# Kernel tuning notes

Hardware: AMD Instinct MI355X
Metric: run time of the kernel (lower is better)

## Reference

```python
import jax, jax.numpy as jnp
import numpy as np
import math

F = 64        # num_features (multiplicity of each irrep)
N = 16000     # nodes
E = 256000    # edges (avg_num_neighbors = 16)
S = 4         # num_species
DE = 32       # scalar edge feature dim (radial basis)
W = 128       # interaction_mlp_width
AVG_NEIGH = 16.0
SQ2 = math.sqrt(2.0)
SQ3 = math.sqrt(3.0)


def setup_inputs() -> dict:
    key = jax.random.key(0)
    ks = jax.random.split(key, 32)
    def nrm(k, shape, scale=1.0):
        return jax.random.normal(k, shape, dtype=jnp.float32) * scale
    inp = {}
    # forward args
    inp["vectors"] = nrm(ks[0], (E, 1, 3))
    inp["lengths"] = jax.random.uniform(ks[1], (E, 1), dtype=jnp.float32)
    inp["node_s"] = nrm(ks[2], (N, F))            # 64x0e part of node_feats
    inp["node_v"] = nrm(ks[3], (N, F, 3))         # 64x1o part of node_feats
    inp["scalar_edge_feats"] = nrm(ks[4], (E, DE))
    inp["node_specie"] = jax.random.randint(ks[5], (N,), 0, S)
    inp["senders"] = jax.random.randint(ks[6], (E,), 0, N)
    inp["receivers"] = jax.random.randint(ks[7], (E,), 0, N)
    # parameters (e3nn Linear = per-irrep channel mixing, fan-in normalized; bias only on 0e)
    inp["W_up_s"] = nrm(ks[8], (F, F), F ** -0.5); inp["b_up_s"] = jnp.zeros((F,), jnp.float32)
    inp["W_up_v"] = nrm(ks[9], (F, F), F ** -0.5)
    din = 2 * F + DE + 1
    inp["mlp_W1"] = nrm(ks[10], (din, W), din ** -0.5); inp["mlp_b1"] = jnp.zeros((W,), jnp.float32)
    inp["mlp_W2"] = nrm(ks[11], (W, W), W ** -0.5); inp["mlp_b2"] = jnp.zeros((W,), jnp.float32)
    inp["mlp_W3"] = nrm(ks[12], (W, 3 * F), W ** -0.5); inp["mlp_b3"] = jnp.zeros((3 * F,), jnp.float32)
    inp["W_dn_s"] = nrm(ks[13], (F, F), F ** -0.5); inp["b_dn_s"] = jnp.zeros((F,), jnp.float32)
    inp["W_dn_v"] = nrm(ks[14], (2 * F, F), (2 * F) ** -0.5)
    # symmetric contraction weights (per species, per channel); correlation=2
    inp["w_sc_s"] = nrm(ks[15], (S, 3, F), 3 ** -0.5)   # paths to 0e: x0, x0^2, (x1.x1)/sqrt3
    inp["w_sc_v"] = nrm(ks[16], (S, 2, F), 2 ** -0.5)   # paths to 1o: x1, x0*x1
    inp["W_pb_s"] = nrm(ks[17], (F, F), F ** -0.5); inp["b_pb_s"] = jnp.zeros((F,), jnp.float32)
    inp["W_pb_v"] = nrm(ks[18], (F, F), F ** -0.5)
    inp["W_r1_s"] = nrm(ks[19], (F, 2 * F), F ** -0.5); inp["b_r1_s"] = jnp.zeros((2 * F,), jnp.float32)
    inp["W_r1_v"] = nrm(ks[20], (F, F), F ** -0.5)
    inp["W_r2_s"] = nrm(ks[21], (F, 1), F ** -0.5); inp["b_r2"] = jnp.zeros((1,), jnp.float32)
    inp["W_r2_v"] = nrm(ks[22], (F, 1), F ** -0.5)
    return inp


def reference(vectors, lengths, node_s, node_v, scalar_edge_feats, node_specie,
              senders, receivers,
              W_up_s, b_up_s, W_up_v,
              mlp_W1, mlp_b1, mlp_W2, mlp_b2, mlp_W3, mlp_b3,
              W_dn_s, b_dn_s, W_dn_v,
              w_sc_s, w_sc_v, W_pb_s, b_pb_s, W_pb_v,
              W_r1_s, b_r1_s, W_r1_v, W_r2_s, b_r2, W_r2_v):
    n = node_s.shape[0]
    # --- spherical harmonics, sh_irreps='1o', component normalization, normalize=False ---
    edge_v = SQ3 * vectors[:, 0, :]                              # [E,3]

    # --- InteractionBlock: linear_up ---
    h_s = node_s @ W_up_s + b_up_s                               # [N,F]
    h_v = jnp.einsum('nfi,fg->ngi', node_v, W_up_v)              # [N,F,3]

    # --- MessagePassingConvolution ---
    m_s = h_s[senders]                                           # [E,F] 0e
    m_v = h_v[senders]                                           # [E,F,3] 1o
    # tensor product with edge 1o, filtered to 0e+1o (unitary CG):
    tp_s = jnp.einsum('efi,ei->ef', m_v, edge_v) / SQ3           # 1o x 1o -> 0e  [E,F]
    tp_v1 = m_s[:, :, None] * edge_v[:, None, :]                 # 0e x 1o -> 1o  [E,F,3]
    tp_v2 = jnp.cross(m_v, edge_v[:, None, :]) / SQ2             # 1o x 1o -> 1o  [E,F,3]
    # scalar MLP mix (one scalar weight per output irrep = 3F)
    mlp_in = jnp.concatenate([m_s, h_s[receivers], scalar_edge_feats, lengths], axis=1)
    h = jax.nn.silu(mlp_in @ mlp_W1 + mlp_b1)
    h = jax.nn.silu(h @ mlp_W2 + mlp_b2)
    mix = h @ mlp_W3 + mlp_b3                                    # [E,3F]
    mix_s, mix_v1, mix_v2 = mix[:, :F], mix[:, F:2 * F], mix[:, 2 * F:]
    tp_s = tp_s * mix_s
    tp_v = jnp.concatenate([tp_v1 * mix_v1[:, :, None], tp_v2 * mix_v2[:, :, None]], axis=1)  # [E,2F,3]
    # scatter-add to receivers, normalize by avg_num_neighbors
    agg_s = jax.ops.segment_sum(tp_s, receivers, num_segments=n) / AVG_NEIGH   # [N,F]
    agg_v = jax.ops.segment_sum(tp_v, receivers, num_segments=n) / AVG_NEIGH   # [N,2F,3]
    # linear_down
    f_s = agg_s @ W_dn_s + b_dn_s                                # [N,F]
    f_v = jnp.einsum('nfi,fg->ngi', agg_v, W_dn_v)               # [N,F,3]

    # --- EquivariantProductBasisBlock: symmetric contraction (correlation=2), per-species ---
    ws = w_sc_s[node_specie]                                     # [N,3,F]
    wv = w_sc_v[node_specie]                                     # [N,2,F]
    vv = jnp.sum(f_v * f_v, axis=-1) / SQ3                       # 1o (x) 1o -> 0e, symmetric
    sc_s = ws[:, 0] * f_s + ws[:, 1] * (f_s * f_s) + ws[:, 2] * vv           # [N,F]
    sc_v = wv[:, 0][:, :, None] * f_v + wv[:, 1][:, :, None] * (f_s[:, :, None] * f_v)  # [N,F,3]
    p_s = sc_s @ W_pb_s + b_pb_s                                 # node_feats 0e out
    p_v = jnp.einsum('nfi,fg->ngi', sc_v, W_pb_v)                # node_feats 1o out

    # --- NonLinearReadoutBlock: linear to (2F x 0e + F x 1o), gate, linear to 1x0e+1x1o ---
    r_s = p_s @ W_r1_s + b_r1_s                                  # [N,2F]
    r_v = jnp.einsum('nfi,fg->ngi', p_v, W_r1_v)                 # [N,F,3]
    act = jax.nn.silu(r_s[:, :F])
    gates = jax.nn.silu(r_s[:, F:])
    g_v = gates[:, :, None] * r_v                                # gated vectors
    out_s = act @ W_r2_s + b_r2                                  # [N,1]  0e output
    out_v = jnp.einsum('nfi,fo->noi', g_v, W_r2_v)               # [N,1,3] 1o output
    return out_s, out_v, p_s, p_v
```

## Files before the change

kernel.cpp:

```cpp
#include <hip/hip_runtime.h>

typedef short bf16x8 __attribute__((ext_vector_type(8)));
typedef float f32x4  __attribute__((ext_vector_type(4)));
typedef unsigned short ushort_t;

__device__ __forceinline__ float silu(float x) {
    float t = __expf(-x);
    return x * __builtin_amdgcn_rcpf(1.f + t);
}

__device__ __forceinline__ ushort_t f2bs(float x) {
    union { float f; unsigned int u; } v; v.f = x;
    unsigned int r = v.u + 0x7FFF + ((v.u >> 16) & 1);
    return (ushort_t)(r >> 16);
}
__device__ __forceinline__ ushort_t f2bs_t(float x) {
    union { float f; unsigned int u; } v; v.f = x;
    return (ushort_t)(v.u >> 16);
}
__device__ __forceinline__ float bs2f(ushort_t x) {
    union { unsigned int u; float f; } v; v.u = ((unsigned int)x) << 16; return v.f;
}

constexpr int N_   = 16000;
constexpr int E_   = 256000;
constexpr int Fd   = 64;

constexpr float SQ3f    = 1.7320508075688772f;
constexpr float INV_SQ3 = 0.5773502691896258f;
constexpr float INV_SQ2 = 0.7071067811865476f;
constexpr float INV_AVG = 0.0625f;

constexpr int OFF_OS = 0;
constexpr int OFF_OV = N_;
constexpr int OFF_PS = OFF_OV + 3 * N_;
constexpr int OFF_PV = OFF_PS + N_ * Fd;

constexpr int W1P_SZ = 6 * 8 * 512;
constexpr int W2P_SZ = 4 * 8 * 512;
constexpr int W3P_SZ = 4 * 12 * 512;

__global__ __launch_bounds__(256) void pack_kernel(
    const float* __restrict__ W1, const float* __restrict__ W2,
    const float* __restrict__ W3,
    ushort_t* __restrict__ W1p, ushort_t* __restrict__ W2p,
    ushort_t* __restrict__ W3p)
{
    int idx = blockIdx.x * 256 + threadIdx.x;
    if (idx < W1P_SZ) {
        int j = idx & 7, lane = (idx >> 3) & 63, tile = idx >> 9;
        int c = tile >> 3, t = tile & 7;
        int k = c * 32 + (lane >> 4) * 8 + j;
        int n = t * 16 + (lane & 15);
        W1p[idx] = f2bs(k < 161 ? W1[k * 128 + n] : 0.f);
    } else if (idx < W1P_SZ + W2P_SZ) {
        int q = idx - W1P_SZ;
        int j = q & 7, lane = (q >> 3) & 63, tile = q >> 9;
        int c = tile >> 3, t = tile & 7;
        int k = c * 32 + (lane >> 4) * 8 + j;
        int n = t * 16 + (lane & 15);
        W2p[q] = f2bs(W2[k * 128 + n]);
    } else {
        int q = idx - W1P_SZ - W2P_SZ;
        int j = q & 7, lane = (q >> 3) & 63, tile = q >> 9;
        int c = tile / 12, t = tile % 12;
        int k = c * 32 + (lane >> 4) * 8 + j;
        int n = t * 16 + (lane & 15);
        W3p[q] = f2bs(W3[k * 192 + n]);
    }
}

__global__ __launch_bounds__(64, 4) void up_kernel(
    const float* __restrict__ node_s, const float* __restrict__ node_v,
    const float* __restrict__ W_up_s, const float* __restrict__ b_up_s,
    const float* __restrict__ W_up_v,
    const int* __restrict__ receivers, int* __restrict__ cnt,
    ushort_t* __restrict__ hs_bf, float* __restrict__ h_v)
{
    __shared__ float ns[4][64];
    __shared__ float nv[4][64][3];
    const int n0 = blockIdx.x * 4;
    const int g  = threadIdx.x;

    {
        int e = blockIdx.x * 64 + g;
        atomicAdd(&cnt[receivers[e]], 1);
    }

    #pragma unroll
    for (int j = 0; j < 4; j++) ns[j][g] = node_s[(n0 + j) * 64 + g];
    for (int idx = g; idx < 4 * 192; idx += 64) {
        int j = idx / 192, r = idx - j * 192;
        nv[j][r / 3][r % 3] = node_v[(size_t)n0 * 192 + idx];
    }
    __syncthreads();

    float as[4], a0[4], a1[4], a2[4];
    float bb = b_up_s[g];
    #pragma unroll
    for (int j = 0; j < 4; j++) { as[j] = bb; a0[j] = a1[j] = a2[j] = 0.f; }
    #pragma unroll 4
    for (int f = 0; f < 64; f++) {
        float wss = W_up_s[f * 64 + g];
        float wv  = W_up_v[f * 64 + g];
        #pragma unroll
        for (int j = 0; j < 4; j++) {
            as[j] += ns[j][f] * wss;
            a0[j] += nv[j][f][0] * wv;
            a1[j] += nv[j][f][1] * wv;
            a2[j] += nv[j][f][2] * wv;
        }
    }
    #pragma unroll
    for (int j = 0; j < 4; j++) {
        hs_bf[(n0 + j) * 64 + g] = f2bs(as[j]);
        h_v[(n0 + j) * 192 + 0 * 64 + g] = a0[j];
        h_v[(n0 + j) * 192 + 1 * 64 + g] = a1[j];
        h_v[(n0 + j) * 192 + 2 * 64 + g] = a2[j];
    }
}

__global__ __launch_bounds__(1024) void scan_kernel(
    const int* __restrict__ cnt, int* __restrict__ base, int* __restrict__ cursor)
{
    __shared__ int part[1024];
    const int t = threadIdx.x;
    int v[16];
    int s = 0;
    if (t < 1000) {
        const int4* c4 = (const int4*)(cnt + t * 16);
        #pragma unroll
        for (int q = 0; q < 4; q++) {
            int4 w = c4[q];
            v[q * 4 + 0] = w.x; v[q * 4 + 1] = w.y;
            v[q * 4 + 2] = w.z; v[q * 4 + 3] = w.w;
            s += w.x + w.y + w.z + w.w;
        }
    }
    part[t] = s;
    __syncthreads();
    for (int off = 1; off < 1024; off <<= 1) {
        int u = (t >= off) ? part[t - off] : 0;
        __syncthreads();
        part[t] += u;
        __syncthreads();
    }
    if (t < 1000) {
        int run = part[t] - s;
        int b[16];
        #pragma unroll
        for (int i = 0; i < 16; i++) { b[i] = run; run += v[i]; }
        int4* bb = (int4*)(base + t * 16);
        int4* cc = (int4*)(cursor + t * 16);
        #pragma unroll
        for (int q = 0; q < 4; q++) {
            int4 w = { b[q * 4], b[q * 4 + 1], b[q * 4 + 2], b[q * 4 + 3] };
            bb[q] = w;
            cc[q] = w;
        }
    }
}

__global__ __launch_bounds__(256, 3) void edge_mlp_kernel(
    const float* __restrict__ lengths, const float* __restrict__ sef,
    const int* __restrict__ senders, const int* __restrict__ receivers,
    const float* __restrict__ b1f, const float* __restrict__ b2f,
    const float* __restrict__ b3f,
    const ushort_t* __restrict__ hs_bf,
    const ushort_t* __restrict__ W1p, const ushort_t* __restrict__ W2p,
    const ushort_t* __restrict__ W3p,
    int* __restrict__ cursor, int* __restrict__ sorted_eid,
    ushort_t* __restrict__ tpx)
{
    __shared__ ushort_t Als[64 * 200];
    __shared__ ushort_t Hs[64 * 136];

    const int tid  = threadIdx.x;
    const int wave = tid >> 6, lane = tid & 63;
    const int quad = lane >> 4, l4 = lane & 15;
    const int e0   = blockIdx.x * 64;

    if (tid < 64) {
        int e = e0 + tid;
        int p = atomicAdd(&cursor[receivers[e]], 1);
        sorted_eid[p] = e;
    }

    {
        const int e  = tid & 63;
        const int ge = e0 + e;
        const int snd = senders[ge];
        const int rcv = receivers[ge];
        for (int c = tid >> 6; c < 24; c += 4) {
            bf16x8 v;
            if (c < 8) {
                v = *(const bf16x8*)(hs_bf + snd * 64 + c * 8);
            } else if (c < 16) {
                v = *(const bf16x8*)(hs_bf + rcv * 64 + (c - 8) * 8);
            } else if (c < 20) {
                const float4 s0 = *(const float4*)(sef + (size_t)ge * 32 + (c - 16) * 8);
                const float4 s1 = *(const float4*)(sef + (size_t)ge * 32 + (c - 16) * 8 + 4);
                v[0] = (short)f2bs(s0.x); v[1] = (short)f2bs(s0.y);
                v[2] = (short)f2bs(s0.z); v[3] = (short)f2bs(s0.w);
                v[4] = (short)f2bs(s1.x); v[5] = (short)f2bs(s1.y);
                v[6] = (short)f2bs(s1.z); v[7] = (short)f2bs(s1.w);
            } else if (c == 20) {
                v = (bf16x8){0,0,0,0,0,0,0,0};
                v[0] = (short)f2bs(lengths[ge]);
            } else {
                v = (bf16x8){0,0,0,0,0,0,0,0};
            }
            *(bf16x8*)(&Als[e * 200 + c * 8]) = v;
        }
    }
    __syncthreads();

    const bf16x8* B1 = (const bf16x8*)W1p;
    const bf16x8* B2 = (const bf16x8*)W2p;
    const bf16x8* B3 = (const bf16x8*)W3p;

    {
        f32x4 acc[2][4];
        #pragma unroll
        for (int ti = 0; ti < 2; ti++)
            #pragma unroll
            for (int m = 0; m < 4; m++) acc[ti][m] = (f32x4){0,0,0,0};
        #pragma unroll
        for (int c = 0; c < 6; c++) {
            bf16x8 b0 = B1[(c * 8 + wave * 2 + 0) * 64 + lane];
            bf16x8 b1 = B1[(c * 8 + wave * 2 + 1) * 64 + lane];
            #pragma unroll
            for (int m = 0; m < 4; m++) {
                bf16x8 a = *(const bf16x8*)(&Als[(m * 16 + l4) * 200 + c * 32 + quad * 8]);
                acc[0][m] = __builtin_amdgcn_mfma_f32_16x16x32_bf16(a, b0, acc[0][m], 0, 0, 0);
                acc[1][m] = __builtin_amdgcn_mfma_f32_16x16x32_bf16(a, b1, acc[1][m], 0, 0, 0);
            }
        }
        #pragma unroll
        for (int ti = 0; ti < 2; ti++) {
            int t = wave * 2 + ti;
            float bb = b1f[t * 16 + l4];
            #pragma unroll
            for (int m = 0; m < 4; m++)
                #pragma unroll
                for (int r = 0; r < 4; r++)
                    Hs[(m * 16 + quad * 4 + r) * 136 + t * 16 + l4] =
                        f2bs_t(silu(acc[ti][m][r] + bb));
        }
    }
    __syncthreads();

    {
        f32x4 acc[2][4];
        #pragma unroll
        for (int ti = 0; ti < 2; ti++)
            #pragma unroll
            for (int m = 0; m < 4; m++) acc[ti][m] = (f32x4){0,0,0,0};
        #pragma unroll
        for (int c = 0; c < 4; c++) {
            bf16x8 b0 = B2[(c * 8 + wave * 2 + 0) * 64 + lane];
            bf16x8 b1 = B2[(c * 8 + wave * 2 + 1) * 64 + lane];
            #pragma unroll
            for (int m = 0; m < 4; m++) {
                bf16x8 a = *(const bf16x8*)(&Hs[(m * 16 + l4) * 136 + c * 32 + quad * 8]);
                acc[0][m] = __builtin_amdgcn_mfma_f32_16x16x32_bf16(a, b0, acc[0][m], 0, 0, 0);
                acc[1][m] = __builtin_amdgcn_mfma_f32_16x16x32_bf16(a, b1, acc[1][m], 0, 0, 0);
            }
        }
        #pragma unroll
        for (int ti = 0; ti < 2; ti++) {
            int t = wave * 2 + ti;
            float bb = b2f[t * 16 + l4];
            #pragma unroll
            for (int m = 0; m < 4; m++)
                #pragma unroll
                for (int r = 0; r < 4; r++)
                    Als[(m * 16 + quad * 4 + r) * 136 + t * 16 + l4] =
                        f2bs_t(silu(acc[ti][m][r] + bb));
        }
    }
    __syncthreads();

    {
        f32x4 acc[3][4];
        #pragma unroll
        for (int ti = 0; ti < 3; ti++)
            #pragma unroll
            for (int m = 0; m < 4; m++) acc[ti][m] = (f32x4){0,0,0,0};
        #pragma unroll
        for (int c = 0; c < 4; c++) {
            bf16x8 b0 = B3[(c * 12 + wave * 3 + 0) * 64 + lane];
            bf16x8 b1 = B3[(c * 12 + wave * 3 + 1) * 64 + lane];
            bf16x8 b2 = B3[(c * 12 + wave * 3 + 2) * 64 + lane];
            #pragma unroll
            for (int m = 0; m < 4; m++) {
                bf16x8 a = *(const bf16x8*)(&Als[(m * 16 + l4) * 136 + c * 32 + quad * 8]);
                acc[0][m] = __builtin_amdgcn_mfma_f32_16x16x32_bf16(a, b0, acc[0][m], 0, 0, 0);
                acc[1][m] = __builtin_amdgcn_mfma_f32_16x16x32_bf16(a, b1, acc[1][m], 0, 0, 0);
                acc[2][m] = __builtin_amdgcn_mfma_f32_16x16x32_bf16(a, b2, acc[2][m], 0, 0, 0);
            }
        }
        #pragma unroll
        for (int ti = 0; ti < 3; ti++) {
            int t = wave * 3 + ti;
            float bb = b3f[t * 16 + l4];
            #pragma unroll
            for (int m = 0; m < 4; m++)
                #pragma unroll
                for (int r = 0; r < 4; r++)
                    tpx[(size_t)(e0 + m * 16 + quad * 4 + r) * 192 + t * 16 + l4] =
                        f2bs(acc[ti][m][r] + bb);
        }
    }
}

__global__ __launch_bounds__(256, 2) void node_fused_kernel(
    const int* __restrict__ base, const int* __restrict__ cnt,
    const int* __restrict__ sorted_eid, const int* __restrict__ senders,
    const float* __restrict__ vectors,
    const ushort_t* __restrict__ tpx,
    const ushort_t* __restrict__ hs_bf, const float* __restrict__ h_v,
    const int* __restrict__ specie,
    const float* __restrict__ W_dn_s, const float* __restrict__ b_dn_s,
    const float* __restrict__ W_dn_v,
    const float* __restrict__ w_sc_s, const float* __restrict__ w_sc_v,
    const float* __restrict__ W_pb_s, const float* __restrict__ b_pb_s,
    const float* __restrict__ W_pb_v,
    const float* __restrict__ W_r1_s, const float* __restrict__ b_r1_s,
    const float* __restrict__ W_r1_v,
    const float* __restrict__ W_r2_s, const float* __restrict__ b_r2,
    const float* __restrict__ W_r2_v,
    float* __restrict__ out)
{
    __shared__ float as_l[4][64];
    __shared__ float av_l[4][128][3];
    __shared__ float scs[4][64];
    __shared__ float scv[4][64][3];
    __shared__ float ps_[4][64];
    __shared__ float pv_[4][64][3];
    __shared__ int   eids[4][64];

    const int tid = threadIdx.x;
    const int w   = tid >> 6;
    const int g   = tid & 63;
    const int n   = blockIdx.x * 4 + w;

    const int b = base[n];
    const int c = cnt[n];
    float accSa = 0.f, accSb = 0.f;
    float a10a = 0.f, a11a = 0.f, a12a = 0.f;
    float a20a = 0.f, a21a = 0.f, a22a = 0.f;
    float a10b = 0.f, a11b = 0.f, a12b = 0.f;
    float a20b = 0.f, a21b = 0.f, a22b = 0.f;

    for (int done = 0; done < c; done += 64) {
        int m = min(64, c - done);
        if (g < m) eids[w][g] = sorted_eid[b + done + g];
        int i = 0;
        for (; i + 1 < m; i += 2) {
            const int e1 = eids[w][i];
            const int e2 = eids[w][i + 1];
            const int se1 = senders[e1];
            const int se2 = senders[e2];
            const float ev10 = SQ3f * vectors[e1 * 3 + 0];
            const float ev11 = SQ3f * vectors[e1 * 3 + 1];
            const float ev12 = SQ3f * vectors[e1 * 3 + 2];
            const float ev20 = SQ3f * vectors[e2 * 3 + 0];
            const float ev21 = SQ3f * vectors[e2 * 3 + 1];
            const float ev22 = SQ3f * vectors[e2 * 3 + 2];
            const float m10 = h_v[(size_t)se1 * 192 + 0 * 64 + g];
            const float m11 = h_v[(size_t)se1 * 192 + 1 * 64 + g];
            const float m12 = h_v[(size_t)se1 * 192 + 2 * 64 + g];
            const float m20 = h_v[(size_t)se2 * 192 + 0 * 64 + g];
            const float m21 = h_v[(size_t)se2 * 192 + 1 * 64 + g];
            const float m22 = h_v[(size_t)se2 * 192 + 2 * 64 + g];
            const float ms1 = bs2f(hs_bf[se1 * 64 + g]);
            const float ms2 = bs2f(hs_bf[se2 * 64 + g]);
            const ushort_t* r1 = tpx + (size_t)e1 * 192;
            const ushort_t* r2 = tpx + (size_t)e2 * 192;
            const float c10 = bs2f(r1[g]), c11 = bs2f(r1[64 + g]), c12 = bs2f(r1[128 + g]);
            const float c20 = bs2f(r2[g]), c21 = bs2f(r2[64 + g]), c22 = bs2f(r2[128 + g]);

            accSa += (m10 * ev10 + m11 * ev11 + m12 * ev12) * c10;
            accSb += (m20 * ev20 + m21 * ev21 + m22 * ev22) * c20;
            float k1a = ms1 * c11, k1b = ms2 * c21;
            a10a += k1a * ev10; a11a += k1a * ev11; a12a += k1a * ev12;
            a10b += k1b * ev20; a11b += k1b * ev21; a12b += k1b * ev22;
            a20a += (m11 * ev12 - m12 * ev11) * c12;
            a21a += (m12 * ev10 - m10 * ev12) * c12;
            a22a += (m10 * ev11 - m11 * ev10) * c12;
            a20b += (m21 * ev22 - m22 * ev21) * c22;
            a21b += (m22 * ev20 - m20 * ev22) * c22;
            a22b += (m20 * ev21 - m21 * ev20) * c22;
        }
        if (i < m) {
            const int e1 = eids[w][i];
            const int se1 = senders[e1];
            const float ev10 = SQ3f * vectors[e1 * 3 + 0];
            const float ev11 = SQ3f * vectors[e1 * 3 + 1];
            const float ev12 = SQ3f * vectors[e1 * 3 + 2];
            const float m10 = h_v[(size_t)se1 * 192 + 0 * 64 + g];
            const float m11 = h_v[(size_t)se1 * 192 + 1 * 64 + g];
            const float m12 = h_v[(size_t)se1 * 192 + 2 * 64 + g];
            const float ms1 = bs2f(hs_bf[se1 * 64 + g]);
            const ushort_t* r1 = tpx + (size_t)e1 * 192;
            const float c10 = bs2f(r1[g]), c11 = bs2f(r1[64 + g]), c12 = bs2f(r1[128 + g]);
            accSa += (m10 * ev10 + m11 * ev11 + m12 * ev12) * c10;
            float k1a = ms1 * c11;
            a10a += k1a * ev10; a11a += k1a * ev11; a12a += k1a * ev12;
            a20a += (m11 * ev12 - m12 * ev11) * c12;
            a21a += (m12 * ev10 - m10 * ev12) * c12;
            a22a += (m10 * ev11 - m11 * ev10) * c12;
        }
    }
    as_l[w][g] = (accSa + accSb) * (INV_SQ3 * INV_AVG);
    av_l[w][g][0] = (a10a + a10b) * INV_AVG;
    av_l[w][g][1] = (a11a + a11b) * INV_AVG;
    av_l[w][g][2] = (a12a + a12b) * INV_AVG;
    av_l[w][64 + g][0] = (a20a + a20b) * (INV_SQ2 * INV_AVG);
    av_l[w][64 + g][1] = (a21a + a21b) * (INV_SQ2 * INV_AVG);
    av_l[w][64 + g][2] = (a22a + a22b) * (INV_SQ2 * INV_AVG);

    float f_s = b_dn_s[g];
    #pragma unroll 8
    for (int f = 0; f < 64; f++) f_s += as_l[w][f] * W_dn_s[f * 64 + g];
    float fv0 = 0.f, fv1 = 0.f, fv2 = 0.f;
    #pragma unroll 8
    for (int f = 0; f < 128; f++) {
        float wt = W_dn_v[f * 64 + g];
        fv0 += av_l[w][f][0] * wt;
        fv1 += av_l[w][f][1] * wt;
        fv2 += av_l[w][f][2] * wt;
    }

    float vv = (fv0 * fv0 + fv1 * fv1 + fv2 * fv2) * INV_SQ3;
    int sp = specie[n];
    float ws0 = w_sc_s[sp * 192 + 0 * 64 + g];
    float ws1 = w_sc_s[sp * 192 + 1 * 64 + g];
    float ws2 = w_sc_s[sp * 192 + 2 * 64 + g];
    float wv0 = w_sc_v[sp * 128 + 0 * 64 + g];
    float wv1 = w_sc_v[sp * 128 + 1 * 64 + g];
    float sc_s = ws0 * f_s + ws1 * f_s * f_s + ws2 * vv;
    float kv = wv0 + wv1 * f_s;
    scs[w][g] = sc_s;
    scv[w][g][0] = kv * fv0;
    scv[w][g][1] = kv * fv1;
    scv[w][g][2] = kv * fv2;

    float p_s = b_pb_s[g];
    float pv0 = 0.f, pv1 = 0.f, pv2 = 0.f;
    #pragma unroll 8
    for (int f = 0; f < 64; f++) {
        float wps = W_pb_s[f * 64 + g];
        p_s += scs[w][f] * wps;
        float wpv = W_pb_v[f * 64 + g];
        pv0 += scv[w][f][0] * wpv;
        pv1 += scv[w][f][1] * wpv;
        pv2 += scv[w][f][2] * wpv;
    }
    ps_[w][g] = p_s;
    pv_[w][g][0] = pv0; pv_[w][g][1] = pv1; pv_[w][g][2] = pv2;

    out[OFF_PS + n * 64 + g] = p_s;
    out[OFF_PV + (size_t)n * 192 + g * 3 + 0] = pv0;
    out[OFF_PV + (size_t)n * 192 + g * 3 + 1] = pv1;
    out[OFF_PV + (size_t)n * 192 + g * 3 + 2] = pv2;

    float r0 = b_r1_s[g];
    float r1 = b_r1_s[g + 64];
    float rv0 = 0.f, rv1 = 0.f, rv2 = 0.f;
    #pragma unroll 8
    for (int f = 0; f < 64; f++) {
        float p = ps_[w][f];
        r0 += p * W_r1_s[f * 128 + g];
        r1 += p * W_r1_s[f * 128 + g + 64];
        float wrv = W_r1_v[f * 64 + g];
        rv0 += pv_[w][f][0] * wrv;
        rv1 += pv_[w][f][1] * wrv;
        rv2 += pv_[w][f][2] * wrv;
    }
    float act  = silu(r0);
    float gate = silu(r1);
    float o_s = act * W_r2_s[g];
    float wr2v = W_r2_v[g];
    float ov0 = gate * rv0 * wr2v;
    float ov1 = gate * rv1 * wr2v;
    float ov2 = gate * rv2 * wr2v;

    #pragma unroll
    for (int off = 32; off > 0; off >>= 1) {
        o_s += __shfl_down(o_s, off);
        ov0 += __shfl_down(ov0, off);
        ov1 += __shfl_down(ov1, off);
        ov2 += __shfl_down(ov2, off);
    }
    if (g == 0) {
        out[OFF_OS + n] = o_s + b_r2[0];
        out[OFF_OV + n * 3 + 0] = ov0;
        out[OFF_OV + n * 3 + 1] = ov1;
        out[OFF_OV + n * 3 + 2] = ov2;
    }
}

extern "C" void kernel_launch(void* const* d_in, const int* in_sizes, int n_in,
                              void* d_out, int out_size, void* d_ws, size_t ws_size,
                              hipStream_t stream)
{
    const float* vectors  = (const float*)d_in[0];
    const float* lengths  = (const float*)d_in[1];
    const float* node_s   = (const float*)d_in[2];
    const float* node_v   = (const float*)d_in[3];
    const float* sef      = (const float*)d_in[4];
    const int*  specie    = (const int*)d_in[5];
    const int*  senders   = (const int*)d_in[6];
    const int*  receivers = (const int*)d_in[7];
    const float* W_up_s   = (const float*)d_in[8];
    const float* b_up_s   = (const float*)d_in[9];
    const float* W_up_v   = (const float*)d_in[10];
    const float* mlp_W1   = (const float*)d_in[11];
    const float* mlp_b1   = (const float*)d_in[12];
    const float* mlp_W2   = (const float*)d_in[13];
    const float* mlp_b2   = (const float*)d_in[14];
    const float* mlp_W3   = (const float*)d_in[15];
    const float* mlp_b3   = (const float*)d_in[16];
    const float* W_dn_s   = (const float*)d_in[17];
    const float* b_dn_s   = (const float*)d_in[18];
    const float* W_dn_v   = (const float*)d_in[19];
    const float* w_sc_s   = (const float*)d_in[20];
    const float* w_sc_v   = (const float*)d_in[21];
    const float* W_pb_s   = (const float*)d_in[22];
    const float* b_pb_s   = (const float*)d_in[23];
    const float* W_pb_v   = (const float*)d_in[24];
    const float* W_r1_s   = (const float*)d_in[25];
    const float* b_r1_s   = (const float*)d_in[26];
    const float* W_r1_v   = (const float*)d_in[27];
    const float* W_r2_s   = (const float*)d_in[28];
    const float* b_r2     = (const float*)d_in[29];
    const float* W_r2_v   = (const float*)d_in[30];

    float* h_v = (float*)d_ws;
    ushort_t* tpx   = (ushort_t*)(h_v + (size_t)N_ * 192);
    ushort_t* hs_bf = tpx + (size_t)E_ * 192;
    ushort_t* W1p   = hs_bf + (size_t)N_ * 64;
    ushort_t* W2p   = W1p + W1P_SZ;
    ushort_t* W3p   = W2p + W2P_SZ;
    int* cnt        = (int*)((((size_t)(W3p + W3P_SZ)) + 15) & ~(size_t)15);
    int* base       = cnt + N_;
    int* cursor     = base + N_;
    int* sorted_eid = cursor + N_;

    float* out = (float*)d_out;

    hipMemsetAsync(cnt, 0, N_ * sizeof(int), stream);

    up_kernel<<<N_ / 4, 64, 0, stream>>>(node_s, node_v, W_up_s, b_up_s, W_up_v,
                                         receivers, cnt, hs_bf, h_v);
    pack_kernel<<<256, 256, 0, stream>>>(mlp_W1, mlp_W2, mlp_W3, W1p, W2p, W3p);
    scan_kernel<<<1, 1024, 0, stream>>>(cnt, base, cursor);

    edge_mlp_kernel<<<E_ / 64, 256, 0, stream>>>(
        lengths, sef, senders, receivers,
        mlp_b1, mlp_b2, mlp_b3,
        hs_bf, W1p, W2p, W3p, cursor, sorted_eid, tpx);

    node_fused_kernel<<<N_ / 4, 256, 0, stream>>>(
        base, cnt, sorted_eid, senders, vectors,
        tpx, hs_bf, h_v, specie,
        W_dn_s, b_dn_s, W_dn_v, w_sc_s, w_sc_v,
        W_pb_s, b_pb_s, W_pb_v, W_r1_s, b_r1_s, W_r1_v,
        W_r2_s, b_r2, W_r2_v, out);
}
```

Baseline: 364.4 us.

## Write edge MLP output and edge metadata in receiver-sorted order

The edge MLP kernel now scatters each edge's tpx row to its receiver-sorted slot, and also writes a packed float4 holding sender index and scaled vector at that slot. The node kernel then reads tpx contiguously by position and loads the metadata with one vector load, avoiding the sorted_eid indirection and the gathers of senders and vectors. The cost is scattered writes of tpx rows from the MLP epilogue plus an extra float4 metadata buffer per edge.

```diff
diff --git a/kernel.cpp b/kernel.cpp
--- a/kernel.cpp
+++ b/kernel.cpp
@@ -164,16 +164,18 @@
 __global__ __launch_bounds__(256, 3) void edge_mlp_kernel(
     const float* __restrict__ lengths, const float* __restrict__ sef,
     const int* __restrict__ senders, const int* __restrict__ receivers,
+    const float* __restrict__ vectors,
     const float* __restrict__ b1f, const float* __restrict__ b2f,
     const float* __restrict__ b3f,
     const ushort_t* __restrict__ hs_bf,
     const ushort_t* __restrict__ W1p, const ushort_t* __restrict__ W2p,
     const ushort_t* __restrict__ W3p,
-    int* __restrict__ cursor, int* __restrict__ sorted_eid,
+    int* __restrict__ cursor, float4* __restrict__ meta,
     ushort_t* __restrict__ tpx)
 {
     __shared__ ushort_t Als[64 * 200];
     __shared__ ushort_t Hs[64 * 136];
+    __shared__ int perm_s[64];
 
     const int tid  = threadIdx.x;
     const int wave = tid >> 6, lane = tid & 63;
@@ -183,7 +185,13 @@
     if (tid < 64) {
         int e = e0 + tid;
         int p = atomicAdd(&cursor[receivers[e]], 1);
-        sorted_eid[p] = e;
+        perm_s[tid] = p;
+        float4 mt;
+        mt.x = __int_as_float(senders[e]);
+        mt.y = SQ3f * vectors[e * 3 + 0];
+        mt.z = SQ3f * vectors[e * 3 + 1];
+        mt.w = SQ3f * vectors[e * 3 + 2];
+        meta[p] = mt;
     }
 
     {
@@ -307,17 +315,17 @@
             #pragma unroll
             for (int m = 0; m < 4; m++)
                 #pragma unroll
-                for (int r = 0; r < 4; r++)
-                    tpx[(size_t)(e0 + m * 16 + quad * 4 + r) * 192 + t * 16 + l4] =
-                        f2bs(acc[ti][m][r] + bb);
+                for (int r = 0; r < 4; r++) {
+                    int p = perm_s[m * 16 + quad * 4 + r];
+                    tpx[(size_t)p * 192 + t * 16 + l4] = f2bs(acc[ti][m][r] + bb);
+                }
         }
     }
 }
 
 __global__ __launch_bounds__(256, 2) void node_fused_kernel(
     const int* __restrict__ base, const int* __restrict__ cnt,
-    const int* __restrict__ sorted_eid, const int* __restrict__ senders,
-    const float* __restrict__ vectors,
+    const float4* __restrict__ meta,
     const ushort_t* __restrict__ tpx,
     const ushort_t* __restrict__ hs_bf, const float* __restrict__ h_v,
     const int* __restrict__ specie,
@@ -338,7 +346,7 @@
     __shared__ float scv[4][64][3];
     __shared__ float ps_[4][64];
     __shared__ float pv_[4][64][3];
-    __shared__ int   eids[4][64];
+    __shared__ float4 lmeta[4][64];
 
     const int tid = threadIdx.x;
     const int w   = tid >> 6;
@@ -355,19 +363,15 @@
 
     for (int done = 0; done < c; done += 64) {
         int m = min(64, c - done);
-        if (g < m) eids[w][g] = sorted_eid[b + done + g];
+        if (g < m) lmeta[w][g] = meta[b + done + g];
         int i = 0;
         for (; i + 1 < m; i += 2) {
-            const int e1 = eids[w][i];
-            const int e2 = eids[w][i + 1];
-            const int se1 = senders[e1];
-            const int se2 = senders[e2];
-            const float ev10 = SQ3f * vectors[e1 * 3 + 0];
-            const float ev11 = SQ3f * vectors[e1 * 3 + 1];
-            const float ev12 = SQ3f * vectors[e1 * 3 + 2];
-            const float ev20 = SQ3f * vectors[e2 * 3 + 0];
-            const float ev21 = SQ3f * vectors[e2 * 3 + 1];
-            const float ev22 = SQ3f * vectors[e2 * 3 + 2];
+            const float4 mt1 = lmeta[w][i];
+            const float4 mt2 = lmeta[w][i + 1];
+            const int se1 = __float_as_int(mt1.x);
+            const int se2 = __float_as_int(mt2.x);
+            const float ev10 = mt1.y, ev11 = mt1.z, ev12 = mt1.w;
+            const float ev20 = mt2.y, ev21 = mt2.z, ev22 = mt2.w;
             const float m10 = h_v[(size_t)se1 * 192 + 0 * 64 + g];
             const float m11 = h_v[(size_t)se1 * 192 + 1 * 64 + g];
             const float m12 = h_v[(size_t)se1 * 192 + 2 * 64 + g];
@@ -376,8 +380,8 @@
             const float m22 = h_v[(size_t)se2 * 192 + 2 * 64 + g];
             const float ms1 = bs2f(hs_bf[se1 * 64 + g]);
             const float ms2 = bs2f(hs_bf[se2 * 64 + g]);
-            const ushort_t* r1 = tpx + (size_t)e1 * 192;
-            const ushort_t* r2 = tpx + (size_t)e2 * 192;
+            const ushort_t* r1 = tpx + (size_t)(b + done + i) * 192;
+            const ushort_t* r2 = r1 + 192;
             const float c10 = bs2f(r1[g]), c11 = bs2f(r1[64 + g]), c12 = bs2f(r1[128 + g]);
             const float c20 = bs2f(r2[g]), c21 = bs2f(r2[64 + g]), c22 = bs2f(r2[128 + g]);
 
@@ -394,16 +398,14 @@
             a22b += (m20 * ev21 - m21 * ev20) * c22;
         }
         if (i < m) {
-            const int e1 = eids[w][i];
-            const int se1 = senders[e1];
-            const float ev10 = SQ3f * vectors[e1 * 3 + 0];
-            const float ev11 = SQ3f * vectors[e1 * 3 + 1];
-            const float ev12 = SQ3f * vectors[e1 * 3 + 2];
+            const float4 mt1 = lmeta[w][i];
+            const int se1 = __float_as_int(mt1.x);
+            const float ev10 = mt1.y, ev11 = mt1.z, ev12 = mt1.w;
             const float m10 = h_v[(size_t)se1 * 192 + 0 * 64 + g];
             const float m11 = h_v[(size_t)se1 * 192 + 1 * 64 + g];
             const float m12 = h_v[(size_t)se1 * 192 + 2 * 64 + g];
             const float ms1 = bs2f(hs_bf[se1 * 64 + g]);
-            const ushort_t* r1 = tpx + (size_t)e1 * 192;
+            const ushort_t* r1 = tpx + (size_t)(b + done + i) * 192;
             const float c10 = bs2f(r1[g]), c11 = bs2f(r1[64 + g]), c12 = bs2f(r1[128 + g]);
             accSa += (m10 * ev10 + m11 * ev11 + m12 * ev12) * c10;
             float k1a = ms1 * c11;
@@ -544,10 +546,10 @@
     ushort_t* W1p   = hs_bf + (size_t)N_ * 64;
     ushort_t* W2p   = W1p + W1P_SZ;
     ushort_t* W3p   = W2p + W2P_SZ;
-    int* cnt        = (int*)((((size_t)(W3p + W3P_SZ)) + 15) & ~(size_t)15);
+    float4* meta    = (float4*)((((size_t)(W3p + W3P_SZ)) + 15) & ~(size_t)15);
+    int* cnt        = (int*)(meta + E_);
     int* base       = cnt + N_;
     int* cursor     = base + N_;
-    int* sorted_eid = cursor + N_;
 
     float* out = (float*)d_out;
 
@@ -559,12 +561,12 @@
     scan_kernel<<<1, 1024, 0, stream>>>(cnt, base, cursor);
 
     edge_mlp_kernel<<<E_ / 64, 256, 0, stream>>>(
-        lengths, sef, senders, receivers,
+        lengths, sef, senders, receivers, vectors,
         mlp_b1, mlp_b2, mlp_b3,
-        hs_bf, W1p, W2p, W3p, cursor, sorted_eid, tpx);
+        hs_bf, W1p, W2p, W3p, cursor, meta, tpx);
 
     node_fused_kernel<<<N_ / 4, 256, 0, stream>>>(
-        base, cnt, sorted_eid, senders, vectors,
+        base, cnt, meta,
         tpx, hs_bf, h_v, specie,
         W_dn_s, b_dn_s, W_dn_v, w_sc_s, w_sc_v,
         W_pb_s, b_pb_s, W_pb_v, W_r1_s, b_r1_s, W_r1_v,
```

Result: no change. 364.4 us (-0.0%).
